# Kernel optimization log

Measured on AMD Instinct MI355X. Metric: run time of the kernel, lower is better.

Reference implementation:

```python
import jax, jax.numpy as jnp
import numpy as np

KAPPA = -1.0          # negative curvature (Poincare ball, c = 1)
EPS = 1e-10
N, D_IN, D_OUT = 8192, 512, 512


def _artan_k(x):
    sc = np.sqrt(-KAPPA)
    return jnp.arctanh(jnp.clip(sc * x, -1.0 + 1e-7, 1.0 - 1e-7)) / sc


def _tan_k(x):
    sc = np.sqrt(-KAPPA)
    return jnp.tanh(sc * x) / sc


def _clamp_abs(x, eps=EPS):
    return jnp.where(x >= 0, 1.0, -1.0) * jnp.maximum(jnp.abs(x), eps)


def _norm(x):
    # stable last-dim L2 norm, clamped away from zero
    return jnp.sqrt(jnp.maximum(jnp.sum(x * x, axis=-1, keepdims=True), EPS * EPS))


def mobius_matvec(W, x):
    # geoopt-style Mobius matrix-vector product: scale x@W so that the
    # gyro-norm matches tan_k((|mx|/|x|) * artan_k(|x|))
    x_norm = _norm(x)                       # [N,1]
    mx = x @ W                              # [N,D_out]
    mx_norm = _norm(mx)
    res = _tan_k(mx_norm / x_norm * _artan_k(x_norm)) * (mx / mx_norm)
    return jnp.where(mx_norm <= EPS, 0.0, res)


def mobius_scalar_mul(r, x):
    x_norm = _norm(x)
    return _tan_k(r * _artan_k(x_norm)) * (x / x_norm)


def weighted_midpoint_lincomb(A, X):
    # weighted Frechet-mean-like midpoint with lincomb=True (geoopt semantics):
    # gamma_i = lambda_x = 2 / (1 + kappa * |x_i|^2)
    gamma = jnp.maximum(2.0 / (1.0 + KAPPA * jnp.sum(X * X, axis=-1, keepdims=True)), 1e-15)  # [N,1]
    denom = _clamp_abs(A @ (gamma - 1.0))   # [N,1]  (sum_j A_ij (gamma_j - 1))
    nom = A @ (gamma * X)                   # [N,D]  (sum_j A_ij gamma_j x_j)  -- GEMM, no NxNxD temp
    two_mean = nom / denom
    sq = jnp.sum(two_mean * two_mean, axis=-1, keepdims=True)
    a_mean = two_mean / (1.0 + jnp.sqrt(jnp.maximum(1.0 + KAPPA * sq, EPS)))
    alpha = jnp.sum(A, axis=-1, keepdims=True)   # lincomb: Mobius-scale by total weight
    return mobius_scalar_mul(alpha, a_mean)


def logmap0(x):
    xn = _norm(x)
    return _artan_k(xn) * x / xn


def expmap0(u):
    un = _norm(u)
    return _tan_k(un) * u / un


def setup_inputs() -> dict:
    key = jax.random.key(0)
    k1, k2, k3 = jax.random.split(key, 3)
    # node embeddings well inside the Poincare ball (|x| ~ 0.02)
    X = jax.random.normal(k1, (N, D_IN), dtype=jnp.float32) * 0.001
    # dense nonnegative normalized adjacency (rows sum ~ 0.5)
    A_hat = jax.random.uniform(k2, (N, N), dtype=jnp.float32) / N
    W = jax.random.normal(k3, (D_IN, D_OUT), dtype=jnp.float32) * 0.01
    return {"X": X, "A_hat": A_hat, "W": W}


def reference(X, A_hat, W):
    XW = mobius_matvec(W, X)                     # Mobius linear layer
    AXW = weighted_midpoint_lincomb(A_hat, XW)   # adjacency-weighted midpoint aggregation
    return expmap0(jax.nn.relu(logmap0(AXW)))    # sigma = exp0(relu(log0(.)))
```

## Files before the change

kernel.cpp:

```cpp
#include <hip/hip_runtime.h>


#define NR 8192
#define DD 512

typedef unsigned int u32;
typedef unsigned short u16;
typedef __attribute__((ext_vector_type(8))) short bf16x8;
typedef __attribute__((ext_vector_type(4))) float f32x4;

__device__ __forceinline__ u16 f2bf(float f) {
  u32 u = __float_as_uint(f);
  u32 r = u + 0x7FFFu + ((u >> 16) & 1u);
  return (u16)(r >> 16);
}

__device__ __forceinline__ u32 cvtpk(float lo, float hi) {
  u32 r;
  asm("v_cvt_pk_bf16_f32 %0, %1, %2" : "=v"(r) : "v"(lo), "v"(hi));
  return r;
}

__device__ __forceinline__ void gload16(const void* g, void* l) {
  __builtin_amdgcn_global_load_lds(
      (const __attribute__((address_space(1))) u32*)g,
      (__attribute__((address_space(3))) u32*)l, 16, 0, 0);
}

__device__ __forceinline__ float wred(float v) {
  #pragma unroll
  for (int off = 32; off; off >>= 1) v += __shfl_xor(v, off, 64);
  return v;
}

__global__ __launch_bounds__(256) void conv_wt(const float* __restrict__ W,
                                               u16* __restrict__ Wt) {
  const int idx = blockIdx.x * 256 + threadIdx.x;
  const int n  = idx >> 6;
  const int k0 = (idx & 63) * 8;
  u32 r[4];
  #pragma unroll
  for (int j = 0; j < 4; ++j) {
    float lo = W[(size_t)(k0 + 2*j    ) * DD + n];
    float hi = W[(size_t)(k0 + 2*j + 1) * DD + n];
    r[j] = (u32)f2bf(lo) | ((u32)f2bf(hi) << 16);
  }
  const int dst = n * DD + ((idx & 63) >> 2) * 32 + (((idx & 3) ^ (n & 3)) * 8);
  *(uint4*)(Wt + dst) = *(const uint4*)r;
}

template <int DOSUM>
__global__ __launch_bounds__(256) void gemm_f32a(
    const float* __restrict__ Af, const u16* __restrict__ Bt,
    const u16* __restrict__ g1bf,
    float* __restrict__ C0, float* __restrict__ Cext,
    float* __restrict__ denp, float* __restrict__ alp,
    int M, int N, int K, int kchunk, int ntm) {
  __shared__ __align__(16) float ldsA[2][4096];
  __shared__ __align__(16) u16   ldsB[2][4096];
  __shared__ __align__(16) u16   ldsG[2048];
  const int p  = blockIdx.x;
  const int q  = (p >> 5) * 8 + (p & 7);
  const int nt = (p >> 3) & 3;
  const int mt = q % ntm;
  const int kc = q / ntm;

  const int t = threadIdx.x;
  const int lane = t & 63, w = t >> 6;
  const int wm = w >> 1, wn = w & 1;
  const int m0 = mt * 128, n0 = nt * 128;
  const int kbeg = kc * kchunk;
  const int lr = lane & 15, lk = lane >> 4, lr3 = lr & 3, lx = lr & 7;
  const bool doRS = DOSUM && (nt == 0);

  const int Rb   = t >> 3;
  const int scol = ((t & 7) ^ (Rb & 7)) << 2;
  const float* gA0 = Af + (size_t)(m0 + Rb) * K + kbeg + scol;
  const size_t apg = (size_t)32 * K;

  const u16* gB = Bt + (size_t)(n0 + (t >> 2)) * K + kbeg + (t & 3) * 8;
  const size_t rstepB = (size_t)64 * K;

  f32x4 acc[4][4];
  #pragma unroll
  for (int i = 0; i < 4; ++i)
    #pragma unroll
    for (int j = 0; j < 4; ++j) acc[i][j] = (f32x4){0.f, 0.f, 0.f, 0.f};
  f32x4 accS[4];
  #pragma unroll
  for (int i = 0; i < 4; ++i) accS[i] = (f32x4){0.f, 0.f, 0.f, 0.f};

  const int nT = kchunk / 32;

  if (doRS) gload16(g1bf + kbeg + w * 512, &ldsG[w * 512]);
  #pragma unroll
  for (int j = 0; j < 4; ++j)
    gload16(gA0 + j * apg, &ldsA[0][w * 256 + j * 1024]);
  gload16(gB,          &ldsB[0][w * 512]);
  gload16(gB + rstepB, &ldsB[0][2048 + w * 512]);
  __syncthreads();

  for (int tt = 0; tt < nT; ++tt) {
    const int cur = tt & 1, nxt = cur ^ 1;
    if (tt + 1 < nT) {
      const int ko = (tt + 1) * 32;
      #pragma unroll
      for (int j = 0; j < 4; ++j)
        gload16(gA0 + ko + j * apg, &ldsA[nxt][w * 256 + j * 1024]);
      gload16(gB + ko,          &ldsB[nxt][w * 512]);
      gload16(gB + ko + rstepB, &ldsB[nxt][2048 + w * 512]);
    }
    bf16x8 af[4], bv[4];
    #pragma unroll
    for (int i = 0; i < 4; ++i) {
      const int rbase = (wm * 64 + i * 16 + lr) * 32;
      f32x4 lo = *(const f32x4*)&ldsA[cur][rbase + (((2*lk    ) ^ lx) << 2)];
      f32x4 hi = *(const f32x4*)&ldsA[cur][rbase + (((2*lk + 1) ^ lx) << 2)];
      union { u32 u[4]; bf16x8 v; } pk;
      pk.u[0] = cvtpk(lo.x, lo.y); pk.u[1] = cvtpk(lo.z, lo.w);
      pk.u[2] = cvtpk(hi.x, hi.y); pk.u[3] = cvtpk(hi.z, hi.w);
      af[i] = pk.v;
      const int rb = (wn * 64 + i * 16 + lr) * 32 + ((lk ^ lr3) << 3);
      bv[i] = *(const bf16x8*)&ldsB[cur][rb];
    }
    #pragma unroll
    for (int mi = 0; mi < 4; ++mi)
      #pragma unroll
      for (int ni = 0; ni < 4; ++ni)
        acc[mi][ni] = __builtin_amdgcn_mfma_f32_16x16x32_bf16(
            af[mi], bv[ni], acc[mi][ni], 0, 0, 0);
    if (doRS && wn == 0) {
      bf16x8 gv;
      if (lr == 0) {
        gv = *(const bf16x8*)&ldsG[tt * 32 + lk * 8];
      } else {
        const short s = (lr == 1) ? (short)0x3F80 : (short)0;
        gv = (bf16x8){s, s, s, s, s, s, s, s};
      }
      #pragma unroll
      for (int i = 0; i < 4; ++i)
        accS[i] = __builtin_amdgcn_mfma_f32_16x16x32_bf16(
            af[i], gv, accS[i], 0, 0, 0);
    }
    __syncthreads();
  }

  if (doRS && wn == 0 && lr < 2) {
    float* dst = ((lr == 0) ? denp : alp) + (size_t)kc * M + m0 + wm * 64;
    #pragma unroll
    for (int i = 0; i < 4; ++i)
      #pragma unroll
      for (int v = 0; v < 4; ++v)
        dst[i * 16 + lk * 4 + v] = accS[i][v];
  }

  float* C = (kc == 0) ? C0 : (Cext + (size_t)(kc - 1) * M * N);
  float* Cw = C + (size_t)(m0 + wm * 64 + lk * 4) * N + n0 + wn * 64 + lr;
  #pragma unroll
  for (int mi = 0; mi < 4; ++mi)
    #pragma unroll
    for (int ni = 0; ni < 4; ++ni)
      #pragma unroll
      for (int v = 0; v < 4; ++v)
        Cw[(size_t)(mi * 16 + v) * N + ni * 16] = acc[mi][ni][v];
}

__global__ __launch_bounds__(256) void rowstats(const float* __restrict__ X,
                                                const float* __restrict__ mx,
                                                float* __restrict__ fg,
                                                u16* __restrict__ g1bf) {
  const int row  = (blockIdx.x << 2) + (threadIdx.x >> 6);
  const int lane = threadIdx.x & 63;
  const float* xr = X  + (size_t)row * DD + lane * 8;
  const float* mr = mx + (size_t)row * DD + lane * 8;
  float4 a0 = *(const float4*)xr, a1 = *(const float4*)(xr + 4);
  float4 b0 = *(const float4*)mr, b1 = *(const float4*)(mr + 4);
  float sx = a0.x*a0.x + a0.y*a0.y + a0.z*a0.z + a0.w*a0.w
           + a1.x*a1.x + a1.y*a1.y + a1.z*a1.z + a1.w*a1.w;
  float sm = b0.x*b0.x + b0.y*b0.y + b0.z*b0.z + b0.w*b0.w
           + b1.x*b1.x + b1.y*b1.y + b1.z*b1.z + b1.w*b1.w;
  sx = wred(sx); sm = wred(sm);
  if (lane == 0) {
    float xn  = sqrtf(fmaxf(sx, 1e-20f));
    float mxn = sqrtf(fmaxf(sm, 1e-20f));
    float at  = atanhf(fminf(xn, 0.9999999f));
    float t_  = tanhf(mxn / xn * at);
    bool  z   = (mxn <= 1e-10f);
    float factor = z ? 0.f : t_ / mxn;
    float xwsq   = z ? 0.f : t_ * t_ * (sm / (mxn * mxn));
    float g = 2.f / (1.f - xwsq);
    g = fmaxf(g, 1e-15f);
    fg[row] = factor * g;
    g1bf[row] = f2bf(g - 1.f);
  }
}

__global__ __launch_bounds__(256) void build_bt(const float* __restrict__ mx,
                                                const float* __restrict__ fg,
                                                u16* __restrict__ Bt) {
  __shared__ float tile[64][65];
  const int j0 = blockIdx.x * 64, d0 = blockIdx.y * 64;
  const int t = threadIdx.x;
  const int r0 = t >> 4, c4 = (t & 15) * 4;
  #pragma unroll
  for (int p = 0; p < 4; ++p) {
    const int r = r0 + p * 16;
    const float s = fg[j0 + r];
    float4 v = *(const float4*)&mx[(size_t)(j0 + r) * DD + d0 + c4];
    tile[r][c4 + 0] = s * v.x; tile[r][c4 + 1] = s * v.y;
    tile[r][c4 + 2] = s * v.z; tile[r][c4 + 3] = s * v.w;
  }
  __syncthreads();
  const int dr = t >> 2, jc = (t & 3) * 16;
  u32 r[8];
  #pragma unroll
  for (int u = 0; u < 8; ++u) {
    float lo = tile[jc + 2 * u][dr];
    float hi = tile[jc + 2 * u + 1][dr];
    r[u] = (u32)f2bf(lo) | ((u32)f2bf(hi) << 16);
  }
  const int s0 = (jc >> 3) & 3;
  const int px = dr & 3;
  u32* rowp = (u32*)(Bt + (size_t)(d0 + dr) * NR + j0 + (jc & 32));
  *(uint4*)(rowp + ((s0 ^ px) * 4))       = *(const uint4*)&r[0];
  *(uint4*)(rowp + (((s0 + 1) ^ px) * 4)) = *(const uint4*)&r[4];
}

__global__ __launch_bounds__(256) void epilogue(const float* __restrict__ P0,
                                                const float* __restrict__ P1,
                                                const float* __restrict__ P2,
                                                const float* __restrict__ P3,
                                                const float* __restrict__ denp,
                                                const float* __restrict__ alp,
                                                float* __restrict__ out) {
  const int row  = (blockIdx.x << 2) + (threadIdx.x >> 6);
  const int lane = threadIdx.x & 63;
  const size_t ro = (size_t)row * DD + lane * 8;
  float4 n0 = *(const float4*)(P0 + ro), n1 = *(const float4*)(P0 + ro + 4);
  float4 a, b;
  a = *(const float4*)(P1 + ro); b = *(const float4*)(P1 + ro + 4);
  n0.x += a.x; n0.y += a.y; n0.z += a.z; n0.w += a.w;
  n1.x += b.x; n1.y += b.y; n1.z += b.z; n1.w += b.w;
  a = *(const float4*)(P2 + ro); b = *(const float4*)(P2 + ro + 4);
  n0.x += a.x; n0.y += a.y; n0.z += a.z; n0.w += a.w;
  n1.x += b.x; n1.y += b.y; n1.z += b.z; n1.w += b.w;
  a = *(const float4*)(P3 + ro); b = *(const float4*)(P3 + ro + 4);
  n0.x += a.x; n0.y += a.y; n0.z += a.z; n0.w += a.w;
  n1.x += b.x; n1.y += b.y; n1.z += b.z; n1.w += b.w;

  float de = 0.f, alpha = 0.f;
  #pragma unroll
  for (int kc = 0; kc < 4; ++kc) {
    de    += denp[kc * NR + row];
    alpha += alp [kc * NR + row];
  }
  de = (de >= 0.f ? 1.f : -1.f) * fmaxf(fabsf(de), 1e-10f);

  float v[8] = {n0.x / de, n0.y / de, n0.z / de, n0.w / de,
                n1.x / de, n1.y / de, n1.z / de, n1.w / de};
  float sq = 0.f;
  #pragma unroll
  for (int j = 0; j < 8; ++j) sq += v[j] * v[j];
  sq = wred(sq);
  float s1 = 1.f + sqrtf(fmaxf(1.f - sq, 1e-10f));
  float an = sqrtf(fmaxf(sq / (s1 * s1), 1e-20f));
  float t2 = tanhf(alpha * atanhf(fminf(an, 0.9999999f)));
  float f2 = t2 / (an * s1);
  float xsq = f2 * f2 * sq;
  float xn = sqrtf(fmaxf(xsq, 1e-20f));
  float lf = atanhf(fminf(xn, 0.9999999f)) / xn;
  float u[8]; float us = 0.f;
  #pragma unroll
  for (int j = 0; j < 8; ++j) {
    u[j] = fmaxf(lf * f2 * v[j], 0.f);
    us += u[j] * u[j];
  }
  us = wred(us);
  float un = sqrtf(fmaxf(us, 1e-20f));
  float ef = tanhf(un) / un;
  float o[8];
  #pragma unroll
  for (int j = 0; j < 8; ++j) o[j] = ef * u[j];
  float* orow = out + (size_t)row * DD + lane * 8;
  *(float4*)orow       = (float4){o[0], o[1], o[2], o[3]};
  *(float4*)(orow + 4) = (float4){o[4], o[5], o[6], o[7]};
}

extern "C" void kernel_launch(void* const* d_in, const int* in_sizes, int n_in,
                              void* d_out, int out_size, void* d_ws, size_t ws_size,
                              hipStream_t stream) {
  const float* X = (const float*)d_in[0];
  const float* A = (const float*)d_in[1];
  const float* W = (const float*)d_in[2];
  float* out = (float*)d_out;
  char* ws = (char*)d_ws;

  float* mx   = (float*)(ws);
  float* Pext = (float*)(ws + 16777216);
  u16*   Bt   = (u16*)(ws + 67108864);
  u16*   Wt   = (u16*)(ws + 75497472);
  float* fg   = (float*)(ws + 76021760);
  u16*   g1bf = (u16*)(ws + 76054528);
  float* denp = (float*)(ws + 76087296);
  float* alp  = (float*)(ws + 76218368);

  const size_t MNf = (size_t)NR * DD;

  conv_wt<<<128, 256, 0, stream>>>(W, Wt);
  gemm_f32a<0><<<256, 256, 0, stream>>>(X, Wt, g1bf, mx, mx, denp, alp,
                                        NR, DD, DD, DD, 64);
  rowstats<<<2048, 256, 0, stream>>>(X, mx, fg, g1bf);
  build_bt<<<dim3(128, 8), 256, 0, stream>>>(mx, fg, Bt);
  gemm_f32a<1><<<1024, 256, 0, stream>>>(A, Bt, g1bf, mx, Pext, denp, alp,
                                         NR, DD, NR, NR / 4, 64);
  epilogue<<<2048, 256, 0, stream>>>(mx, Pext, Pext + MNf, Pext + 2 * MNf,
                                     denp, alp, out);
}
```

Before: 218.5 us.

## Widen GEMM tiles to full output width with 512-thread blocks

Both GEMMs now use 512-thread blocks whose 128-row tile covers all 512 output columns. Each fp32 A tile (including the large adjacency matrix) is streamed from memory once per row tile instead of once per column tile. Each wave holds twice as many accumulators and the B staging buffer in LDS grows fourfold. That adds register and LDS pressure, limiting residency to about one block per CU. The first GEMM drops to only 64 blocks, which may underfill the GPU.

```diff
diff --git a/kernel.cpp b/kernel.cpp
--- a/kernel.cpp
+++ b/kernel.cpp
@@ -50,54 +50,52 @@
 }
 
 template <int DOSUM>
-__global__ __launch_bounds__(256) void gemm_f32a(
+__global__ __launch_bounds__(512, 2) void gemm_big(
     const float* __restrict__ Af, const u16* __restrict__ Bt,
     const u16* __restrict__ g1bf,
     float* __restrict__ C0, float* __restrict__ Cext,
     float* __restrict__ denp, float* __restrict__ alp,
-    int M, int N, int K, int kchunk, int ntm) {
+    int M, int K, int kchunk, int nkc) {
   __shared__ __align__(16) float ldsA[2][4096];
-  __shared__ __align__(16) u16   ldsB[2][4096];
+  __shared__ __align__(16) u16   ldsB[2][16384];
   __shared__ __align__(16) u16   ldsG[2048];
-  const int p  = blockIdx.x;
-  const int q  = (p >> 5) * 8 + (p & 7);
-  const int nt = (p >> 3) & 3;
-  const int mt = q % ntm;
-  const int kc = q / ntm;
+
+  const int bid = blockIdx.x;
+  int mt, kc;
+  if (nkc == 1) { mt = bid; kc = 0; }
+  else { kc = (bid & 7) >> 1; mt = ((bid >> 3) << 1) | (bid & 1); }
 
   const int t = threadIdx.x;
   const int lane = t & 63, w = t >> 6;
-  const int wm = w >> 1, wn = w & 1;
-  const int m0 = mt * 128, n0 = nt * 128;
+  const int wm = w >> 2, wn = w & 3;
+  const int m0 = mt * 128;
   const int kbeg = kc * kchunk;
-  const int lr = lane & 15, lk = lane >> 4, lr3 = lr & 3, lx = lr & 7;
-  const bool doRS = DOSUM && (nt == 0);
+  const int lr = lane & 15, lk = lane >> 4, lx = lr & 7;
 
   const int Rb   = t >> 3;
   const int scol = ((t & 7) ^ (Rb & 7)) << 2;
   const float* gA0 = Af + (size_t)(m0 + Rb) * K + kbeg + scol;
-  const size_t apg = (size_t)32 * K;
-
-  const u16* gB = Bt + (size_t)(n0 + (t >> 2)) * K + kbeg + (t & 3) * 8;
-  const size_t rstepB = (size_t)64 * K;
-
-  f32x4 acc[4][4];
+
+  const u16* gB = Bt + (size_t)(t >> 2) * K + kbeg + (t & 3) * 8;
+
+  f32x4 acc[4][8];
   #pragma unroll
   for (int i = 0; i < 4; ++i)
     #pragma unroll
-    for (int j = 0; j < 4; ++j) acc[i][j] = (f32x4){0.f, 0.f, 0.f, 0.f};
+    for (int j = 0; j < 8; ++j) acc[i][j] = (f32x4){0.f, 0.f, 0.f, 0.f};
   f32x4 accS[4];
   #pragma unroll
   for (int i = 0; i < 4; ++i) accS[i] = (f32x4){0.f, 0.f, 0.f, 0.f};
 
   const int nT = kchunk / 32;
 
-  if (doRS) gload16(g1bf + kbeg + w * 512, &ldsG[w * 512]);
+  if (DOSUM && w < 4) gload16(g1bf + kbeg + t * 8, &ldsG[t * 8]);
+  #pragma unroll
+  for (int j = 0; j < 2; ++j)
+    gload16(gA0 + (size_t)j * 64 * K, &ldsA[0][t * 4 + j * 2048]);
   #pragma unroll
   for (int j = 0; j < 4; ++j)
-    gload16(gA0 + j * apg, &ldsA[0][w * 256 + j * 1024]);
-  gload16(gB,          &ldsB[0][w * 512]);
-  gload16(gB + rstepB, &ldsB[0][2048 + w * 512]);
+    gload16(gB + (size_t)j * 128 * K, &ldsB[0][t * 8 + j * 4096]);
   __syncthreads();
 
   for (int tt = 0; tt < nT; ++tt) {
@@ -105,12 +103,13 @@
     if (tt + 1 < nT) {
       const int ko = (tt + 1) * 32;
       #pragma unroll
+      for (int j = 0; j < 2; ++j)
+        gload16(gA0 + ko + (size_t)j * 64 * K, &ldsA[nxt][t * 4 + j * 2048]);
+      #pragma unroll
       for (int j = 0; j < 4; ++j)
-        gload16(gA0 + ko + j * apg, &ldsA[nxt][w * 256 + j * 1024]);
-      gload16(gB + ko,          &ldsB[nxt][w * 512]);
-      gload16(gB + ko + rstepB, &ldsB[nxt][2048 + w * 512]);
+        gload16(gB + ko + (size_t)j * 128 * K, &ldsB[nxt][t * 8 + j * 4096]);
     }
-    bf16x8 af[4], bv[4];
+    bf16x8 af[4], bv[8];
     #pragma unroll
     for (int i = 0; i < 4; ++i) {
       const int rbase = (wm * 64 + i * 16 + lr) * 32;
@@ -120,16 +119,19 @@
       pk.u[0] = cvtpk(lo.x, lo.y); pk.u[1] = cvtpk(lo.z, lo.w);
       pk.u[2] = cvtpk(hi.x, hi.y); pk.u[3] = cvtpk(hi.z, hi.w);
       af[i] = pk.v;
-      const int rb = (wn * 64 + i * 16 + lr) * 32 + ((lk ^ lr3) << 3);
+    }
+    #pragma unroll
+    for (int i = 0; i < 8; ++i) {
+      const int rb = (wn * 128 + i * 16 + lr) * 32 + ((lk ^ (lr & 3)) << 3);
       bv[i] = *(const bf16x8*)&ldsB[cur][rb];
     }
     #pragma unroll
     for (int mi = 0; mi < 4; ++mi)
       #pragma unroll
-      for (int ni = 0; ni < 4; ++ni)
+      for (int ni = 0; ni < 8; ++ni)
         acc[mi][ni] = __builtin_amdgcn_mfma_f32_16x16x32_bf16(
             af[mi], bv[ni], acc[mi][ni], 0, 0, 0);
-    if (doRS && wn == 0) {
+    if (DOSUM && wn == 0) {
       bf16x8 gv;
       if (lr == 0) {
         gv = *(const bf16x8*)&ldsG[tt * 32 + lk * 8];
@@ -145,7 +147,7 @@
     __syncthreads();
   }
 
-  if (doRS && wn == 0 && lr < 2) {
+  if (DOSUM && wn == 0 && lr < 2) {
     float* dst = ((lr == 0) ? denp : alp) + (size_t)kc * M + m0 + wm * 64;
     #pragma unroll
     for (int i = 0; i < 4; ++i)
@@ -154,15 +156,15 @@
         dst[i * 16 + lk * 4 + v] = accS[i][v];
   }
 
-  float* C = (kc == 0) ? C0 : (Cext + (size_t)(kc - 1) * M * N);
-  float* Cw = C + (size_t)(m0 + wm * 64 + lk * 4) * N + n0 + wn * 64 + lr;
+  float* C = (kc == 0) ? C0 : (Cext + (size_t)(kc - 1) * M * DD);
+  float* Cw = C + (size_t)(m0 + wm * 64 + lk * 4) * DD + wn * 128 + lr;
   #pragma unroll
   for (int mi = 0; mi < 4; ++mi)
     #pragma unroll
-    for (int ni = 0; ni < 4; ++ni)
+    for (int ni = 0; ni < 8; ++ni)
       #pragma unroll
       for (int v = 0; v < 4; ++v)
-        Cw[(size_t)(mi * 16 + v) * N + ni * 16] = acc[mi][ni][v];
+        Cw[(size_t)(mi * 16 + v) * DD + ni * 16] = acc[mi][ni][v];
 }
 
 __global__ __launch_bounds__(256) void rowstats(const float* __restrict__ X,
@@ -307,12 +309,12 @@
   const size_t MNf = (size_t)NR * DD;
 
   conv_wt<<<128, 256, 0, stream>>>(W, Wt);
-  gemm_f32a<0><<<256, 256, 0, stream>>>(X, Wt, g1bf, mx, mx, denp, alp,
-                                        NR, DD, DD, DD, 64);
+  gemm_big<0><<<64, 512, 0, stream>>>(X, Wt, g1bf, mx, mx, denp, alp,
+                                      NR, DD, DD, 1);
   rowstats<<<2048, 256, 0, stream>>>(X, mx, fg, g1bf);
   build_bt<<<dim3(128, 8), 256, 0, stream>>>(mx, fg, Bt);
-  gemm_f32a<1><<<1024, 256, 0, stream>>>(A, Bt, g1bf, mx, Pext, denp, alp,
-                                         NR, DD, NR, NR / 4, 64);
+  gemm_big<1><<<256, 512, 0, stream>>>(A, Bt, g1bf, mx, Pext, denp, alp,
+                                       NR, NR, NR / 4, 4);
   epilogue<<<2048, 256, 0, stream>>>(mx, Pext, Pext + MNf, Pext + 2 * MNf,
                                      denp, alp, out);
 }
```

Result: no change. 220.7 us (+1.0%).
